# Optimization experiments

Measured on AMD Instinct MI355X. Metric: run time of the kernel, lower is better.

## Reference

```python
import jax, jax.numpy as jnp
import numpy as np

B, H, W, C = 16, 128, 128, 64
UP = 2  # up_size=(2,2)
HO, WO = H * UP, W * UP
FLAT_OUT = HO * WO * C  # per-batch flat output size


def setup_inputs() -> dict:
    key = jax.random.key(0)
    k1, k2, k3 = jax.random.split(key, 3)
    updates = jax.random.normal(k1, (B, H, W, C), dtype=jnp.float32)
    # Realistic max_pool_with_argmax indices: each pooled cell (h, w, c) maps to
    # a random position inside its 2x2 window in the upsampled image:
    #   idx = ((UP*h + dh) * WO + (UP*w + dw)) * C + c
    dh = jax.random.randint(k2, (B, H, W, C), 0, UP)
    dw = jax.random.randint(k3, (B, H, W, C), 0, UP)
    hh = UP * jnp.arange(H)[None, :, None, None] + dh  # [B,H,W,C]
    ww = UP * jnp.arange(W)[None, None, :, None] + dw
    cc = jnp.arange(C)[None, None, None, :]
    mask = ((hh * WO + ww) * C + cc).astype(jnp.int32)
    return {"updates": updates, "mask": mask}


def reference(updates, mask):
    b, h, w, c = updates.shape
    ho, wo = h * UP, w * UP
    pool_flat = updates.reshape(b, h * w * c)           # [B, HWC]
    ind_flat = mask.reshape(b, h * w * c)               # [B, HWC], per-batch flat idx
    out = jnp.zeros((b, ho * wo * c), dtype=updates.dtype)
    # tf.scatter_nd sums duplicate indices -> use .at[].add for faithfulness
    out = out.at[jnp.arange(b)[:, None], ind_flat].add(pool_flat)
    return out.reshape(b, ho, wo, c)
```

## Files before the change

kernel.cpp:

```cpp
#include <hip/hip_runtime.h>


constexpr int B  = 16;
constexpr int H  = 128;
constexpr int W  = 128;
constexpr int C  = 64;
constexpr int UP = 2;
constexpr int HO = H * UP;
constexpr int WO = W * UP;
constexpr int C4 = C / 4;

typedef float f32x4 __attribute__((ext_vector_type(4)));
typedef int   i32x4 __attribute__((ext_vector_type(4)));

__global__ __launch_bounds__(256) void unpool_expand(
    const f32x4* __restrict__ upd,
    const i32x4* __restrict__ msk,
    f32x4*       __restrict__ out)
{
    const int t = blockIdx.x * blockDim.x + threadIdx.x;

    const int c4 = t & (C4 - 1);
    const int w  = (t >> 4) & (W - 1);
    const int h  = (t >> 11) & (H - 1);
    const int b  = t >> 18;

    const f32x4 u = __builtin_nontemporal_load(&upd[t]);
    const i32x4 m = __builtin_nontemporal_load(&msk[t]);

    const int cbase = c4 * 4;
    const long obase = (long)b * ((long)HO * WO * C4);

#pragma unroll
    for (int dh = 0; dh < 2; ++dh) {
#pragma unroll
        for (int dw = 0; dw < 2; ++dw) {
            const int row = 2 * h + dh;
            const int col = 2 * w + dw;
            const int flat0 = (row * WO + col) * C + cbase;
            f32x4 v;
            v.x = (m.x == flat0 + 0) ? u.x : 0.0f;
            v.y = (m.y == flat0 + 1) ? u.y : 0.0f;
            v.z = (m.z == flat0 + 2) ? u.z : 0.0f;
            v.w = (m.w == flat0 + 3) ? u.w : 0.0f;
            __builtin_nontemporal_store(v, &out[obase + (long)(row * WO + col) * C4 + c4]);
        }
    }
}

extern "C" void kernel_launch(void* const* d_in, const int* in_sizes, int n_in,
                              void* d_out, int out_size, void* d_ws, size_t ws_size,
                              hipStream_t stream) {
    const f32x4* upd = (const f32x4*)d_in[0];
    const i32x4* msk = (const i32x4*)d_in[1];
    f32x4*       out = (f32x4*)d_out;

    const int n_threads = B * H * W * C4;
    const int block = 256;
    const int grid  = n_threads / block;

    unpool_expand<<<grid, block, 0, stream>>>(upd, msk, out);
}
```

Measured before the change: 344.5 us.

## Switch unpool from input-driven expand to output-driven gather with contiguous stores

Maps one thread per output vec4 instead of one thread per input vec4 writing four outputs. Each thread computes its source pooled cell and reads updates and mask through regular cached loads, so every input is read four times via cache, and output stores become fully contiguous. The aim is better store coalescing and more threads in flight, at the cost of redundant input loads and four times as many threads.

```diff
diff --git a/kernel.cpp b/kernel.cpp
--- a/kernel.cpp
+++ b/kernel.cpp
@@ -13,39 +13,34 @@
 typedef float f32x4 __attribute__((ext_vector_type(4)));
 typedef int   i32x4 __attribute__((ext_vector_type(4)));
 
-__global__ __launch_bounds__(256) void unpool_expand(
+__global__ __launch_bounds__(256) void unpool_gather(
     const f32x4* __restrict__ upd,
     const i32x4* __restrict__ msk,
     f32x4*       __restrict__ out)
 {
     const int t = blockIdx.x * blockDim.x + threadIdx.x;
 
-    const int c4 = t & (C4 - 1);
-    const int w  = (t >> 4) & (W - 1);
-    const int h  = (t >> 11) & (H - 1);
-    const int b  = t >> 18;
+    const int c4  = t & (C4 - 1);
+    const int col = (t >> 4) & (WO - 1);
+    const int row = (t >> 12) & (HO - 1);
+    const int b   = t >> 20;
 
-    const f32x4 u = __builtin_nontemporal_load(&upd[t]);
-    const i32x4 m = __builtin_nontemporal_load(&msk[t]);
+    const int h = row >> 1;
+    const int w = col >> 1;
+    const int iidx = ((b * H + h) * W + w) * C4 + c4;
 
-    const int cbase = c4 * 4;
-    const long obase = (long)b * ((long)HO * WO * C4);
+    const f32x4 u = upd[iidx];
+    const i32x4 m = msk[iidx];
 
-#pragma unroll
-    for (int dh = 0; dh < 2; ++dh) {
-#pragma unroll
-        for (int dw = 0; dw < 2; ++dw) {
-            const int row = 2 * h + dh;
-            const int col = 2 * w + dw;
-            const int flat0 = (row * WO + col) * C + cbase;
-            f32x4 v;
-            v.x = (m.x == flat0 + 0) ? u.x : 0.0f;
-            v.y = (m.y == flat0 + 1) ? u.y : 0.0f;
-            v.z = (m.z == flat0 + 2) ? u.z : 0.0f;
-            v.w = (m.w == flat0 + 3) ? u.w : 0.0f;
-            __builtin_nontemporal_store(v, &out[obase + (long)(row * WO + col) * C4 + c4]);
-        }
-    }
+    const int flat0 = (row * WO + col) * C + c4 * 4;
+
+    f32x4 v;
+    v.x = (m.x == flat0 + 0) ? u.x : 0.0f;
+    v.y = (m.y == flat0 + 1) ? u.y : 0.0f;
+    v.z = (m.z == flat0 + 2) ? u.z : 0.0f;
+    v.w = (m.w == flat0 + 3) ? u.w : 0.0f;
+
+    __builtin_nontemporal_store(v, &out[t]);
 }
 
 extern "C" void kernel_launch(void* const* d_in, const int* in_sizes, int n_in,
@@ -55,9 +50,9 @@
     const i32x4* msk = (const i32x4*)d_in[1];
     f32x4*       out = (f32x4*)d_out;
 
-    const int n_threads = B * H * W * C4;
+    const int n_threads = B * HO * WO * C4;
     const int block = 256;
     const int grid  = n_threads / block;
 
-    unpool_expand<<<grid, block, 0, stream>>>(upd, msk, out);
+    unpool_gather<<<grid, block, 0, stream>>>(upd, msk, out);
 }
```

New measurement: 344.6 us. About the same (+0.0%).
